# Performance work log

Hardware: AMD Instinct MI355X
Metric: run time of the kernel (lower is better)

## Reference

```python
import jax, jax.numpy as jnp
import numpy as np

SEQ_LEN = 4096
HIDDEN = 1280
NUM_HEADS = 16
HEAD_DIM = HIDDEN // NUM_HEADS  # 80
NUM_SEQS = 8


def setup_inputs() -> dict:
    key = jax.random.key(0)
    ks = jax.random.split(key, 8)
    x = jax.random.normal(ks[0], (SEQ_LEN, HIDDEN), dtype=jnp.float32)
    # rotary tables: use cos/sin of random angles so they are bounded like real RoPE tables
    ang = jax.random.uniform(ks[1], (SEQ_LEN, HEAD_DIM), dtype=jnp.float32) * 6.283185
    cos = jnp.cos(ang)
    sin = jnp.sin(ang)
    # variable-length packed segments: strictly increasing boundaries incl. 0 and SEQ_LEN
    rng = np.random.default_rng(0)
    inner = np.sort(rng.choice(np.arange(1, SEQ_LEN), size=NUM_SEQS - 1, replace=False))
    cu_seqlens = jnp.asarray(np.concatenate([[0], inner, [SEQ_LEN]]), dtype=jnp.int32)
    s = 0.02
    w_qkv = jax.random.normal(ks[2], (HIDDEN, 3 * HIDDEN), dtype=jnp.float32) * s
    b_qkv = jnp.zeros((3 * HIDDEN,), dtype=jnp.float32)
    w_proj = jax.random.normal(ks[3], (HIDDEN, HIDDEN), dtype=jnp.float32) * s
    b_proj = jnp.zeros((HIDDEN,), dtype=jnp.float32)
    return {"x": x, "cu_seqlens": cu_seqlens, "cos": cos, "sin": sin,
            "w_qkv": w_qkv, "b_qkv": b_qkv, "w_proj": w_proj, "b_proj": b_proj}


def _rotate_half(t):
    d = t.shape[-1] // 2
    return jnp.concatenate([-t[..., d:], t[..., :d]], axis=-1)


def _apply_rope(q, k, cos, sin):
    # q,k: (S,H,D); cos,sin: (S,D) broadcast over heads, computed in fp32
    c = cos[:, None, :].astype(jnp.float32)
    s = sin[:, None, :].astype(jnp.float32)
    qf, kf = q.astype(jnp.float32), k.astype(jnp.float32)
    q_out = qf * c + _rotate_half(qf) * s
    k_out = kf * c + _rotate_half(kf) * s
    return q_out.astype(q.dtype), k_out.astype(k.dtype)


def reference(x, cu_seqlens, cos, sin, w_qkv, b_qkv, w_proj, b_proj):
    S = x.shape[0]
    scale = HEAD_DIM ** (-0.5)
    qkv = (x @ w_qkv + b_qkv).reshape(S, 3, NUM_HEADS, HEAD_DIM)
    q, k, v = qkv[:, 0], qkv[:, 1], qkv[:, 2]  # each (S,H,D)
    q, k = _apply_rope(q, k, cos, sin)
    # block-diagonal varlen attention via segment-id mask (same math as per-chunk softmax)
    pos = jnp.arange(S)
    seg = jnp.searchsorted(cu_seqlens[1:], pos, side='right')  # (S,) segment id
    mask = seg[:, None] == seg[None, :]  # (S,S) block-diagonal
    scores = jnp.einsum('shd,thd->hst', q, k) * scale  # (H,S,S)
    scores = jnp.where(mask[None], scores.astype(jnp.float32), jnp.finfo(jnp.float32).min)
    attn = jax.nn.softmax(scores, axis=-1).astype(q.dtype)
    out = jnp.einsum('hst,thd->shd', attn, v).reshape(S, NUM_HEADS * HEAD_DIM)
    return out @ w_proj + b_proj
```

## Files before the change

kernel.cpp:

```cpp
#include <hip/hip_runtime.h>
#include <cstdint>
#include <cstddef>

typedef __bf16 bf16x8 __attribute__((ext_vector_type(8)));
typedef float f32x4 __attribute__((ext_vector_type(4)));
typedef float f32x16 __attribute__((ext_vector_type(16)));

#define SEQ   4096
#define HID   1280
#define NH    16
#define HD    80

__device__ __forceinline__ unsigned short f2bf(float f) {
  unsigned int u = __float_as_uint(f);
  unsigned int r = u + 0x7FFFu + ((u >> 16) & 1u);
  return (unsigned short)(r >> 16);
}
__device__ __forceinline__ float bf2f(unsigned short h) {
  return __uint_as_float(((unsigned int)h) << 16);
}
__device__ __forceinline__ __bf16 us2bf(unsigned short u) {
  union { unsigned short s; __bf16 b; } c; c.s = u; return c.b;
}
__device__ __forceinline__ void dma16(const void* g, void* l) {
  __builtin_amdgcn_global_load_lds((const __attribute__((address_space(1))) unsigned int*)g,
                                   (__attribute__((address_space(3))) unsigned int*)l, 16, 0, 0);
}
__device__ __forceinline__ unsigned int cvtpk(float a, float b) {
  unsigned int w;
  asm("v_cvt_pk_bf16_f32 %0, %1, %2" : "=v"(w) : "v"(a), "v"(b));
  return w;
}
__device__ __forceinline__ float lo2f(unsigned int w) { return __uint_as_float(w << 16); }
__device__ __forceinline__ float hi2f(unsigned int w) { return __uint_as_float(w & 0xffff0000u); }

__global__ __launch_bounds__(256) void split_hi_kernel(const float* __restrict__ x,
                                                       unsigned short* __restrict__ hi,
                                                       int n4) {
  int i = blockIdx.x * 256 + threadIdx.x;
  if (i >= n4) return;
  float4 v = *((const float4*)x + i);
  *((ushort4*)hi + i) = make_ushort4(f2bf(v.x), f2bf(v.y), f2bf(v.z), f2bf(v.w));
}

__global__ __launch_bounds__(256) void tsplit_kernel(const float* __restrict__ W,
                                                     unsigned short* __restrict__ Thi,
                                                     unsigned short* __restrict__ Tlo,
                                                     int K, int N) {
  __shared__ float tile[32][33];
  int n0 = blockIdx.x * 32, k0 = blockIdx.y * 32;
  int tx = threadIdx.x & 31, ty = threadIdx.x >> 5;
#pragma unroll
  for (int i = 0; i < 32; i += 8)
    tile[ty + i][tx] = W[(size_t)(k0 + ty + i) * N + n0 + tx];
  __syncthreads();
#pragma unroll
  for (int i = 0; i < 32; i += 8) {
    float v = tile[tx][ty + i];
    size_t idx = (size_t)(n0 + ty + i) * K + (size_t)(k0 + tx);
    unsigned short h = f2bf(v);
    Thi[idx] = h;
    Tlo[idx] = f2bf(v - bf2f(h));
  }
}

__global__ __launch_bounds__(256, 3) void gemm128_x2(
    const unsigned short* __restrict__ A, const unsigned short* __restrict__ Bh,
    const unsigned short* __restrict__ Bl, const float* __restrict__ bias,
    float* __restrict__ out0, float* __restrict__ out1, float* __restrict__ out2,
    int M, int N, int K) {
  __shared__ __align__(16) unsigned short sALL[3 * 8192];

  const int t = threadIdx.x;
  const int lane = t & 63, wave = t >> 6;
  const int c16 = lane & 15, quad = lane >> 4;
  const int bm = blockIdx.y * 128, bn = blockIdx.x * 128;
  const int wr = (wave >> 1) * 64, wc = (wave & 1) * 64;
  const int lrow = lane >> 3;
  const int lswz = (lane & 7) ^ lrow;

  f32x4 acc[4][4];
#pragma unroll
  for (int i = 0; i < 4; ++i)
#pragma unroll
    for (int j = 0; j < 4; ++j) acc[i][j] = (f32x4){0.f, 0.f, 0.f, 0.f};

  const unsigned short* gp[12];
#pragma unroll
  for (int i = 0; i < 12; ++i) {
    const int ua = wave * 12 + i;
    const int arr = ua >> 4, sub = ua & 15;
    const unsigned short* g = (arr == 0) ? A : (arr == 1) ? Bh : Bl;
    const int rowg = ((arr == 0) ? bm : bn) + sub * 8 + lrow;
    gp[i] = g + (size_t)rowg * K + lswz * 8;
  }

  for (int k0 = 0; k0 < K; k0 += 64) {
    __syncthreads();
#pragma unroll
    for (int i = 0; i < 12; ++i)
      dma16(gp[i] + k0, &sALL[(wave * 12 + i) * 512]);
    __syncthreads();
#pragma unroll
    for (int ks = 0; ks < 2; ++ks) {
      bf16x8 a[4], bh[4], bl[4];
#pragma unroll
      for (int mi = 0; mi < 4; ++mi) {
        const int row = wr + mi * 16 + c16;
        const int off = row * 64 + (((ks * 4 + quad) ^ (row & 7)) * 8);
        a[mi] = *(const bf16x8*)&sALL[off];
      }
#pragma unroll
      for (int ni = 0; ni < 4; ++ni) {
        const int row = wc + ni * 16 + c16;
        const int off = row * 64 + (((ks * 4 + quad) ^ (row & 7)) * 8);
        bh[ni] = *(const bf16x8*)&sALL[8192 + off];
        bl[ni] = *(const bf16x8*)&sALL[16384 + off];
      }
#pragma unroll
      for (int mi = 0; mi < 4; ++mi)
#pragma unroll
        for (int ni = 0; ni < 4; ++ni) {
          acc[mi][ni] = __builtin_amdgcn_mfma_f32_16x16x32_bf16(a[mi], bh[ni], acc[mi][ni], 0, 0, 0);
          acc[mi][ni] = __builtin_amdgcn_mfma_f32_16x16x32_bf16(a[mi], bl[ni], acc[mi][ni], 0, 0, 0);
        }
    }
  }
#pragma unroll
  for (int ni = 0; ni < 4; ++ni) {
    int colg = bn + wc + ni * 16 + c16;
    float bv = bias[colg];
    float* op;
    int c = colg;
    if (c < 1280) op = out0;
    else if (c < 2560) { op = out1; c -= 1280; }
    else { op = out2; c -= 2560; }
#pragma unroll
    for (int mi = 0; mi < 4; ++mi)
#pragma unroll
      for (int r = 0; r < 4; ++r) {
        int rowg = bm + wr + mi * 16 + quad * 4 + r;
        op[(size_t)rowg * 1280 + c] = acc[mi][ni][r] + bv;
      }
  }
}

__global__ __launch_bounds__(256) void rope_pack_kernel(
    float* __restrict__ qf, const float* __restrict__ kf,
    const float* __restrict__ cs, const float* __restrict__ sn,
    unsigned short* __restrict__ khi, unsigned short* __restrict__ klo) {
  const int h = blockIdx.y;
  const int s = blockIdx.x * 64 + (threadIdx.x >> 2);
  const int p = threadIdx.x & 3;
  float* qrow = qf + (size_t)s * HID + h * HD;
  const float* krow = kf + (size_t)s * HID + h * HD;
  const float* cr = cs + (size_t)s * HD;
  const float* sr = sn + (size_t)s * HD;
  unsigned short* kh = khi + ((size_t)h * SEQ + s) * HD;
  unsigned short* kl = klo + ((size_t)h * SEQ + s) * HD;
#pragma unroll
  for (int j = 0; j < 10; ++j) {
    int d = 10 * p + j;
    float c0 = cr[d], s0 = sr[d], c1 = cr[d + 40], s1 = sr[d + 40];
    float q0 = qrow[d], q1 = qrow[d + 40];
    qrow[d]      = q0 * c0 - q1 * s0;
    qrow[d + 40] = q1 * c1 + q0 * s1;
    float k0 = krow[d], k1 = krow[d + 40];
    float kn0 = k0 * c0 - k1 * s0;
    float kn1 = k1 * c1 + k0 * s1;
    unsigned short h0 = f2bf(kn0), h1 = f2bf(kn1);
    kh[d] = h0;      kl[d] = f2bf(kn0 - bf2f(h0));
    kh[d + 40] = h1; kl[d + 40] = f2bf(kn1 - bf2f(h1));
  }
}

__global__ __launch_bounds__(256) void vt_pack_kernel(const float* __restrict__ vf,
                                                      unsigned short* __restrict__ vthi,
                                                      unsigned short* __restrict__ vtlo) {
  __shared__ unsigned short sTh[80][72];
  __shared__ unsigned short sTl[80][72];
  const int h = blockIdx.y;
  const int s0 = blockIdx.x * 64;
  const int t = threadIdx.x;
  {
    int row = t >> 2, p = (t & 3) * 20;
    const float* src = vf + (size_t)(s0 + row) * HID + h * HD + p;
#pragma unroll
    for (int i = 0; i < 5; ++i) {
      float4 v = *(const float4*)(src + 4 * i);
      float vv[4] = {v.x, v.y, v.z, v.w};
#pragma unroll
      for (int j = 0; j < 4; ++j) {
        int d = p + 4 * i + j;
        unsigned short hu = f2bf(vv[j]);
        sTh[d][row] = hu;
        sTl[d][row] = f2bf(vv[j] - bf2f(hu));
      }
    }
  }
  __syncthreads();
  if (t < 160) {
    int d = t >> 1, half = (t & 1) * 32;
    size_t base = (size_t)(h * HD + d) * SEQ + s0 + half;
#pragma unroll
    for (int i = 0; i < 8; ++i) {
      *(ushort4*)&vthi[base + 4 * i] = *(ushort4*)&sTh[d][half + 4 * i];
      *(ushort4*)&vtlo[base + 4 * i] = *(ushort4*)&sTl[d][half + 4 * i];
    }
  }
}

__global__ __launch_bounds__(128) void sched_kernel(const int* __restrict__ cu,
                                                    int* __restrict__ perm,
                                                    unsigned int* __restrict__ ctr) {
  __shared__ int w[128];
  const int t = threadIdx.x;
  if (t < 8) ctr[t * 16] = 0u;
  int cu_r[9];
#pragma unroll
  for (int i = 0; i < 9; ++i) cu_r[i] = cu[i];
  const int r0 = t * 32;
  int sg0 = 0, sg1 = 0;
#pragma unroll
  for (int i = 1; i < 8; ++i) {
    sg0 += (r0      >= cu_r[i]) ? 1 : 0;
    sg1 += (r0 + 31 >= cu_r[i]) ? 1 : 0;
  }
  const int ck0 = cu_r[sg0] & ~31;
  const int kend = cu_r[sg1 + 1];
  w[t] = (kend - ck0 + 31) >> 5;
  __syncthreads();
  const int wt = w[t];
  int rank = 0;
  for (int i = 0; i < 128; ++i)
    rank += ((w[i] > wt) || (w[i] == wt && i < t)) ? 1 : 0;
#pragma unroll
  for (int x = 0; x < 8; ++x) {
    perm[x * 256 + rank * 2 + 0] = (2 * x) * 128 + t;
    perm[x * 256 + rank * 2 + 1] = (2 * x + 1) * 128 + t;
  }
}


#define MFMA32(A, B, C) __builtin_amdgcn_mfma_f32_32x32x16_bf16(A, B, C, 0, 0, 0)

__global__ __launch_bounds__(128, 2) void attn_kernel(
    const float* __restrict__ qf, const unsigned short* __restrict__ khi,
    const unsigned short* __restrict__ klo, const unsigned short* __restrict__ vthi,
    const unsigned short* __restrict__ vtlo, const int* __restrict__ cu,
    unsigned short* __restrict__ ohi, const int* __restrict__ perm,
    unsigned int* __restrict__ ctr) {
  __shared__ __align__(16) unsigned short sAll[20480];

  const int t = threadIdx.x;
  const int lane = t & 63, wave = t >> 6;
  const int ln5 = lane & 31;
  const int hi  = lane >> 5;
  const int ln7 = lane & 7;
  const int xcd = blockIdx.x & 7;

  unsigned short* const wb  = sAll + wave * 10240;
  unsigned short* const sKh = wb;
  unsigned short* const sKl = wb + 2560;
  unsigned short* const sVh = wb + 5120;
  unsigned short* const sVl = wb + 7680;

  int cu_r[9];
#pragma unroll
  for (int i = 0; i < 9; ++i) cu_r[i] = cu[i];

  int koff[5];
#pragma unroll
  for (int i = 0; i < 5; ++i) {
    const int G = i * 64 + lane;
    const int key = (G * 205) >> 11;
    const int p = G - key * 10;
    const int cl = (p < 8) ? (p ^ (key & 7)) : p;
    koff[i] = key * 80 + cl * 8;
  }
  int voff[5];
#pragma unroll
  for (int i = 0; i < 5; ++i) {
    const int G = i * 64 + lane;
    const int d = G >> 2, gc = G & 3;
    const int g = gc ^ ((d >> 1) & 3);
    voff[i] = d * SEQ + g * 8;
  }
  int ccol[5];
#pragma unroll
  for (int c = 0; c < 5; ++c)
    ccol[c] = (c < 4) ? ((((2 * c) + hi) ^ ln7) * 8) : ((8 + hi) * 8);
  int gcol[2];
#pragma unroll
  for (int c = 0; c < 2; ++c)
    gcol[c] = (((2 * c) + hi) ^ ((ln5 >> 1) & 3)) * 8;

  const float qsc = 0.11180339887498949f * 1.4426950408889634f;

  for (;;) {
    unsigned int idx = 0;
    if (lane == 0) idx = atomicAdd(&ctr[xcd * 16], 1u);
    idx = (unsigned int)__shfl((int)idx, 0);
    if (idx >= 256u) break;
    const int uu = perm[xcd * 256 + idx];
    const int h = uu >> 7;
    const int r0 = (uu & 127) * 32;

    const int q_my = r0 + ln5;
    int sq = 0, sg0 = 0, sg1 = 0;
#pragma unroll
    for (int i = 1; i < 8; ++i) {
      sq  += (q_my    >= cu_r[i]) ? 1 : 0;
      sg0 += (r0      >= cu_r[i]) ? 1 : 0;
      sg1 += (r0 + 31 >= cu_r[i]) ? 1 : 0;
    }
    const int kb_lo = cu_r[sq], kb_hi = cu_r[sq + 1];
    const int ck0 = cu_r[sg0] & ~31;
    const int kend = cu_r[sg1 + 1];
    const int nchunk = (kend - ck0 + 31) >> 5;

    bf16x8 qh[5], ql[5];
    {
      const float* qrow = qf + (size_t)q_my * HID + h * HD;
#pragma unroll
      for (int kt = 0; kt < 5; ++kt) {
        const int d0 = kt * 16 + hi * 8;
        float4 a0 = *(const float4*)(qrow + d0);
        float4 a1 = *(const float4*)(qrow + d0 + 4);
        float va[8] = {a0.x, a0.y, a0.z, a0.w, a1.x, a1.y, a1.z, a1.w};
        bf16x8 hf, lf;
#pragma unroll
        for (int j = 0; j < 8; ++j) {
          float v = va[j] * qsc;
          unsigned short hu = f2bf(v);
          hf[j] = us2bf(hu);
          lf[j] = us2bf(f2bf(v - bf2f(hu)));
        }
        qh[kt] = hf; ql[kt] = lf;
      }
    }

    f32x16 O0, O1, O2;
#pragma unroll
    for (int r = 0; r < 16; ++r) { O0[r] = 0.f; O1[r] = 0.f; O2[r] = 0.f; }
    float m_i = -1e30f, l_i = 0.f;

    const unsigned short* gkh = khi + (size_t)h * SEQ * 80;
    const unsigned short* gkl = klo + (size_t)h * SEQ * 80;
    const unsigned short* gvh = vthi + (size_t)h * HD * SEQ;
    const unsigned short* gvl = vtlo + (size_t)h * HD * SEQ;

    {
      const size_t kb = (size_t)ck0 * 80;
#pragma unroll
      for (int i = 0; i < 5; ++i) dma16(gkh + kb + koff[i], sKh + i * 512);
#pragma unroll
      for (int i = 0; i < 5; ++i) dma16(gkl + kb + koff[i], sKl + i * 512);
#pragma unroll
      for (int i = 0; i < 5; ++i) dma16(gvh + ck0 + voff[i], sVh + i * 512);
#pragma unroll
      for (int i = 0; i < 5; ++i) dma16(gvl + ck0 + voff[i], sVl + i * 512);
    }

    for (int ci = 0; ci < nchunk; ++ci) {
      const int ck = ck0 + ci * 32;
      asm volatile("s_waitcnt vmcnt(10)" ::: "memory");

      f32x16 sc;
#pragma unroll
      for (int r = 0; r < 16; ++r) sc[r] = 0.f;
      __builtin_amdgcn_s_setprio(1);
#pragma unroll
      for (int kd = 0; kd < 5; ++kd) {
        const int col = ccol[kd];
        bf16x8 kh = *(const bf16x8*)&sKh[ln5 * 80 + col];
        bf16x8 kl = *(const bf16x8*)&sKl[ln5 * 80 + col];
        sc = MFMA32(kh, qh[kd], sc);
        sc = MFMA32(kh, ql[kd], sc);
        sc = MFMA32(kl, qh[kd], sc);
      }
      __builtin_amdgcn_s_setprio(0);

      __builtin_amdgcn_sched_barrier(0);
      if (ci + 1 < nchunk) {
        const size_t kb = (size_t)(ck + 32) * 80;
#pragma unroll
        for (int i = 0; i < 5; ++i) dma16(gkh + kb + koff[i], sKh + i * 512);
#pragma unroll
        for (int i = 0; i < 5; ++i) dma16(gkl + kb + koff[i], sKl + i * 512);
      }

      float mx = -1e30f;
      {
        const int kb = ck + 4 * hi;
#pragma unroll
        for (int r = 0; r < 16; ++r) {
          const int kg = kb + (r & 3) + 8 * (r >> 2);
          float v = (kg >= kb_lo && kg < kb_hi) ? sc[r] : -1e30f;
          sc[r] = v;
          mx = fmaxf(mx, v);
        }
      }
      mx = fmaxf(mx, __shfl_xor(mx, 32));
      const float mnew = fmaxf(m_i, mx);
      const float alpha = exp2f(m_i - mnew);
      float ps = 0.f;
#pragma unroll
      for (int r = 0; r < 16; ++r) {
        const float s = sc[r];
        const float p = (s > -1e29f) ? exp2f(s - mnew) : 0.f;
        ps += p;
        sc[r] = p;
      }
      ps += __shfl_xor(ps, 32);
      l_i = l_i * alpha + ps;
      m_i = mnew;
#pragma unroll
      for (int r = 0; r < 16; ++r) { O0[r] *= alpha; O1[r] *= alpha; O2[r] *= alpha; }

      if (ci + 1 < nchunk) {
        asm volatile("s_waitcnt vmcnt(10)" ::: "memory");
      } else {
        asm volatile("s_waitcnt vmcnt(0)" ::: "memory");
      }

      __builtin_amdgcn_s_setprio(1);
#pragma unroll
      for (int KT = 0; KT < 2; ++KT) {
        unsigned int A1 = cvtpk(sc[KT * 8 + 0], sc[KT * 8 + 1]);
        unsigned int A2 = cvtpk(sc[KT * 8 + 2], sc[KT * 8 + 3]);
        unsigned int B1 = cvtpk(sc[KT * 8 + 4], sc[KT * 8 + 5]);
        unsigned int B2 = cvtpk(sc[KT * 8 + 6], sc[KT * 8 + 7]);
        float e0 = sc[KT * 8 + 0] - lo2f(A1), e1 = sc[KT * 8 + 1] - hi2f(A1);
        float e2 = sc[KT * 8 + 2] - lo2f(A2), e3 = sc[KT * 8 + 3] - hi2f(A2);
        float e4 = sc[KT * 8 + 4] - lo2f(B1), e5 = sc[KT * 8 + 5] - hi2f(B1);
        float e6 = sc[KT * 8 + 6] - lo2f(B2), e7 = sc[KT * 8 + 7] - hi2f(B2);
        unsigned int C1 = cvtpk(e0, e1), C2 = cvtpk(e2, e3);
        unsigned int D1 = cvtpk(e4, e5), D2 = cvtpk(e6, e7);
        unsigned int T1 = (unsigned int)__shfl_xor((int)(hi ? A1 : B1), 32);
        unsigned int T2 = (unsigned int)__shfl_xor((int)(hi ? A2 : B2), 32);
        unsigned int U1 = (unsigned int)__shfl_xor((int)(hi ? C1 : D1), 32);
        unsigned int U2 = (unsigned int)__shfl_xor((int)(hi ? C2 : D2), 32);
        union { unsigned int w[4]; bf16x8 v; } ph_, pl_;
        ph_.w[0] = hi ? T1 : A1;  ph_.w[1] = hi ? T2 : A2;
        ph_.w[2] = hi ? B1 : T1;  ph_.w[3] = hi ? B2 : T2;
        pl_.w[0] = hi ? U1 : C1;  pl_.w[1] = hi ? U2 : C2;
        pl_.w[2] = hi ? D1 : U1;  pl_.w[3] = hi ? D2 : U2;
        const int vc = gcol[KT];
        bf16x8 vh0 = *(const bf16x8*)&sVh[ln5 * 32 + vc];
        bf16x8 vh1 = *(const bf16x8*)&sVh[(32 + ln5) * 32 + vc];
        bf16x8 vh2 = *(const bf16x8*)&sVh[(64 + (ln5 & 15)) * 32 + vc];
        bf16x8 vl0 = *(const bf16x8*)&sVl[ln5 * 32 + vc];
        bf16x8 vl1 = *(const bf16x8*)&sVl[(32 + ln5) * 32 + vc];
        bf16x8 vl2 = *(const bf16x8*)&sVl[(64 + (ln5 & 15)) * 32 + vc];
        O0 = MFMA32(vh0, ph_.v, O0); O1 = MFMA32(vh1, ph_.v, O1);
        O2 = MFMA32(vh2, ph_.v, O2);
        O0 = MFMA32(vl0, ph_.v, O0); O1 = MFMA32(vl1, ph_.v, O1);
        O2 = MFMA32(vl2, ph_.v, O2);
        O0 = MFMA32(vh0, pl_.v, O0); O1 = MFMA32(vh1, pl_.v, O1);
        O2 = MFMA32(vh2, pl_.v, O2);
      }
      __builtin_amdgcn_s_setprio(0);

      __builtin_amdgcn_sched_barrier(0);
      if (ci + 1 < nchunk) {
        const int cn = ck + 32;
#pragma unroll
        for (int i = 0; i < 5; ++i) dma16(gvh + cn + voff[i], sVh + i * 512);
#pragma unroll
        for (int i = 0; i < 5; ++i) dma16(gvl + cn + voff[i], sVl + i * 512);
      }
    }

    const float inv = 1.0f / l_i;
    unsigned short* orow = ohi + (size_t)q_my * HID + h * HD + 4 * hi;
#pragma unroll
    for (int j = 0; j < 4; ++j) {
      unsigned long long w =
          (unsigned long long)cvtpk(O0[4 * j] * inv, O0[4 * j + 1] * inv) |
          ((unsigned long long)cvtpk(O0[4 * j + 2] * inv, O0[4 * j + 3] * inv) << 32);
      *(unsigned long long*)&orow[8 * j] = w;
    }
#pragma unroll
    for (int j = 0; j < 4; ++j) {
      unsigned long long w =
          (unsigned long long)cvtpk(O1[4 * j] * inv, O1[4 * j + 1] * inv) |
          ((unsigned long long)cvtpk(O1[4 * j + 2] * inv, O1[4 * j + 3] * inv) << 32);
      *(unsigned long long*)&orow[32 + 8 * j] = w;
    }
#pragma unroll
    for (int j = 0; j < 2; ++j) {
      unsigned long long w =
          (unsigned long long)cvtpk(O2[4 * j] * inv, O2[4 * j + 1] * inv) |
          ((unsigned long long)cvtpk(O2[4 * j + 2] * inv, O2[4 * j + 3] * inv) << 32);
      *(unsigned long long*)&orow[64 + 8 * j] = w;
    }
  }
}

extern "C" void kernel_launch(void* const* d_in, const int* in_sizes, int n_in,
                              void* d_out, int out_size, void* d_ws, size_t ws_size,
                              hipStream_t stream) {
  const float* x      = (const float*)d_in[0];
  const int*   cu     = (const int*)d_in[1];
  const float* cs     = (const float*)d_in[2];
  const float* sn     = (const float*)d_in[3];
  const float* w_qkv  = (const float*)d_in[4];
  const float* b_qkv  = (const float*)d_in[5];
  const float* w_proj = (const float*)d_in[6];
  const float* b_proj = (const float*)d_in[7];
  float* out = (float*)d_out;

  char* ws = (char*)d_ws;
  float*          qf     = (float*)(ws + 0);
  float*          kf     = (float*)(ws + 20971520ULL);
  unsigned short* vthi   = (unsigned short*)(ws + 20971520ULL);
  unsigned short* vtlo   = (unsigned short*)(ws + 31457280ULL);
  float*          vf     = (float*)(ws + 41943040ULL);
  unsigned short* o_hi   = (unsigned short*)(ws + 41943040ULL);
  unsigned short* x_hi   = (unsigned short*)(ws + 62914560ULL);
  unsigned short* khi    = (unsigned short*)(ws + 62914560ULL);
  unsigned short* klo    = (unsigned short*)(ws + 73400320ULL);
  unsigned short* wqt_hi = (unsigned short*)(ws + 83886080ULL);
  unsigned short* wqt_lo = (unsigned short*)(ws + 93716480ULL);
  unsigned short* wpt_hi = (unsigned short*)(ws + 103546880ULL);
  unsigned short* wpt_lo = (unsigned short*)(ws + 106823680ULL);
  unsigned int*   ctr    = (unsigned int*)(ws + 83886080ULL);
  int*            perm   = (int*)(ws + 83886080ULL + 1024);

  split_hi_kernel<<<5120, 256, 0, stream>>>(x, x_hi, 1310720);
  tsplit_kernel<<<dim3(120, 40), 256, 0, stream>>>(w_qkv, wqt_hi, wqt_lo, 1280, 3840);
  tsplit_kernel<<<dim3(40, 40), 256, 0, stream>>>(w_proj, wpt_hi, wpt_lo, 1280, 1280);
  gemm128_x2<<<dim3(30, 32), 256, 0, stream>>>(x_hi, wqt_hi, wqt_lo, b_qkv,
                                               qf, kf, vf, 4096, 3840, 1280);
  rope_pack_kernel<<<dim3(64, 16), 256, 0, stream>>>(qf, kf, cs, sn, khi, klo);
  vt_pack_kernel<<<dim3(64, 16), 256, 0, stream>>>(vf, vthi, vtlo);
  sched_kernel<<<1, 128, 0, stream>>>(cu, perm, ctr);
  attn_kernel<<<768, 128, 0, stream>>>(qf, khi, klo, vthi, vtlo, cu, o_hi, perm, ctr);
  gemm128_x2<<<dim3(10, 32), 256, 0, stream>>>(o_hi, wpt_hi, wpt_lo, b_proj,
                                               out, nullptr, nullptr, 4096, 1280, 1280);
}
```

Before: 370.6 us.

## Load V fragments directly from global memory instead of staging in LDS

```diff
diff --git a/kernel.cpp b/kernel.cpp
--- a/kernel.cpp
+++ b/kernel.cpp
@@ -250,7 +250,7 @@
     const unsigned short* __restrict__ vtlo, const int* __restrict__ cu,
     unsigned short* __restrict__ ohi, const int* __restrict__ perm,
     unsigned int* __restrict__ ctr) {
-  __shared__ __align__(16) unsigned short sAll[20480];
+  __shared__ __align__(16) unsigned short sAll[10240];
 
   const int t = threadIdx.x;
   const int lane = t & 63, wave = t >> 6;
@@ -259,11 +259,9 @@
   const int ln7 = lane & 7;
   const int xcd = blockIdx.x & 7;
 
-  unsigned short* const wb  = sAll + wave * 10240;
+  unsigned short* const wb  = sAll + wave * 5120;
   unsigned short* const sKh = wb;
   unsigned short* const sKl = wb + 2560;
-  unsigned short* const sVh = wb + 5120;
-  unsigned short* const sVl = wb + 7680;
 
   int cu_r[9];
 #pragma unroll
@@ -278,22 +276,14 @@
     const int cl = (p < 8) ? (p ^ (key & 7)) : p;
     koff[i] = key * 80 + cl * 8;
   }
-  int voff[5];
-#pragma unroll
-  for (int i = 0; i < 5; ++i) {
-    const int G = i * 64 + lane;
-    const int d = G >> 2, gc = G & 3;
-    const int g = gc ^ ((d >> 1) & 3);
-    voff[i] = d * SEQ + g * 8;
-  }
   int ccol[5];
 #pragma unroll
   for (int c = 0; c < 5; ++c)
     ccol[c] = (c < 4) ? ((((2 * c) + hi) ^ ln7) * 8) : ((8 + hi) * 8);
-  int gcol[2];
-#pragma unroll
-  for (int c = 0; c < 2; ++c)
-    gcol[c] = (((2 * c) + hi) ^ ((ln5 >> 1) & 3)) * 8;
+
+  const size_t vra = (size_t)ln5 * SEQ;
+  const size_t vrb = (size_t)(32 + ln5) * SEQ;
+  const size_t vrc = (size_t)(64 + (ln5 & 15)) * SEQ;
 
   const float qsc = 0.11180339887498949f * 1.4426950408889634f;
 
@@ -356,15 +346,26 @@
       for (int i = 0; i < 5; ++i) dma16(gkh + kb + koff[i], sKh + i * 512);
 #pragma unroll
       for (int i = 0; i < 5; ++i) dma16(gkl + kb + koff[i], sKl + i * 512);
-#pragma unroll
-      for (int i = 0; i < 5; ++i) dma16(gvh + ck0 + voff[i], sVh + i * 512);
-#pragma unroll
-      for (int i = 0; i < 5; ++i) dma16(gvl + ck0 + voff[i], sVl + i * 512);
     }
 
     for (int ci = 0; ci < nchunk; ++ci) {
       const int ck = ck0 + ci * 32;
-      asm volatile("s_waitcnt vmcnt(10)" ::: "memory");
+      asm volatile("s_waitcnt vmcnt(0)" ::: "memory");
+
+      const int k0o = ck + hi * 8;
+      const int k1o = ck + 16 + hi * 8;
+      bf16x8 v0ha = *(const bf16x8*)&gvh[vra + k0o];
+      bf16x8 v0hb = *(const bf16x8*)&gvh[vrb + k0o];
+      bf16x8 v0hc = *(const bf16x8*)&gvh[vrc + k0o];
+      bf16x8 v0la = *(const bf16x8*)&gvl[vra + k0o];
+      bf16x8 v0lb = *(const bf16x8*)&gvl[vrb + k0o];
+      bf16x8 v0lc = *(const bf16x8*)&gvl[vrc + k0o];
+      bf16x8 v1ha = *(const bf16x8*)&gvh[vra + k1o];
+      bf16x8 v1hb = *(const bf16x8*)&gvh[vrb + k1o];
+      bf16x8 v1hc = *(const bf16x8*)&gvh[vrc + k1o];
+      bf16x8 v1la = *(const bf16x8*)&gvl[vra + k1o];
+      bf16x8 v1lb = *(const bf16x8*)&gvl[vrb + k1o];
+      bf16x8 v1lc = *(const bf16x8*)&gvl[vrc + k1o];
 
       f32x16 sc;
 #pragma unroll
@@ -417,12 +418,6 @@
       m_i = mnew;
 #pragma unroll
       for (int r = 0; r < 16; ++r) { O0[r] *= alpha; O1[r] *= alpha; O2[r] *= alpha; }
-
-      if (ci + 1 < nchunk) {
-        asm volatile("s_waitcnt vmcnt(10)" ::: "memory");
-      } else {
-        asm volatile("s_waitcnt vmcnt(0)" ::: "memory");
-      }
 
       __builtin_amdgcn_s_setprio(1);
 #pragma unroll
@@ -446,13 +441,12 @@
         ph_.w[2] = hi ? B1 : T1;  ph_.w[3] = hi ? B2 : T2;
         pl_.w[0] = hi ? U1 : C1;  pl_.w[1] = hi ? U2 : C2;
         pl_.w[2] = hi ? D1 : U1;  pl_.w[3] = hi ? D2 : U2;
-        const int vc = gcol[KT];
-        bf16x8 vh0 = *(const bf16x8*)&sVh[ln5 * 32 + vc];
-        bf16x8 vh1 = *(const bf16x8*)&sVh[(32 + ln5) * 32 + vc];
-        bf16x8 vh2 = *(const bf16x8*)&sVh[(64 + (ln5 & 15)) * 32 + vc];
-        bf16x8 vl0 = *(const bf16x8*)&sVl[ln5 * 32 + vc];
-        bf16x8 vl1 = *(const bf16x8*)&sVl[(32 + ln5) * 32 + vc];
-        bf16x8 vl2 = *(const bf16x8*)&sVl[(64 + (ln5 & 15)) * 32 + vc];
+        bf16x8 vh0 = KT ? v1ha : v0ha;
+        bf16x8 vh1 = KT ? v1hb : v0hb;
+        bf16x8 vh2 = KT ? v1hc : v0hc;
+        bf16x8 vl0 = KT ? v1la : v0la;
+        bf16x8 vl1 = KT ? v1lb : v0lb;
+        bf16x8 vl2 = KT ? v1lc : v0lc;
         O0 = MFMA32(vh0, ph_.v, O0); O1 = MFMA32(vh1, ph_.v, O1);
         O2 = MFMA32(vh2, ph_.v, O2);
         O0 = MFMA32(vl0, ph_.v, O0); O1 = MFMA32(vl1, ph_.v, O1);
@@ -461,15 +455,6 @@
         O2 = MFMA32(vh2, pl_.v, O2);
       }
       __builtin_amdgcn_s_setprio(0);
-
-      __builtin_amdgcn_sched_barrier(0);
-      if (ci + 1 < nchunk) {
-        const int cn = ck + 32;
-#pragma unroll
-        for (int i = 0; i < 5; ++i) dma16(gvh + cn + voff[i], sVh + i * 512);
-#pragma unroll
-        for (int i = 0; i < 5; ++i) dma16(gvl + cn + voff[i], sVl + i * 512);
-      }
     }
 
     const float inv = 1.0f / l_i;
@@ -536,7 +521,7 @@
   rope_pack_kernel<<<dim3(64, 16), 256, 0, stream>>>(qf, kf, cs, sn, khi, klo);
   vt_pack_kernel<<<dim3(64, 16), 256, 0, stream>>>(vf, vthi, vtlo);
   sched_kernel<<<1, 128, 0, stream>>>(cu, perm, ctr);
-  attn_kernel<<<768, 128, 0, stream>>>(qf, khi, klo, vthi, vtlo, cu, o_hi, perm, ctr);
+  attn_kernel<<<1024, 128, 0, stream>>>(qf, khi, klo, vthi, vtlo, cu, o_hi, perm, ctr);
   gemm128_x2<<<dim3(10, 32), 256, 0, stream>>>(o_hi, wpt_hi, wpt_lo, b_proj,
                                                out, nullptr, nullptr, 4096, 1280, 1280);
 }
```

Measured after the change: 414.6 us. +11.9%, slower.
